# Optimization experiments

Hardware: AMD Instinct MI355X
Metric: run time of the kernel (lower is better)

Reference implementation:

```python
import jax, jax.numpy as jnp
import numpy as np
import math

N_QUBITS = 10
N_VQC_LAYERS = 3
N_ACTIONS = 3
B = 4096
T = 128
D = 1 << N_QUBITS
IU, JU = np.triu_indices(N_QUBITS, 1)  # combinations(range(N),2) order


def _ry(a):
    # [B] (or scalar) -> [...,2,2] complex64 RY(a)
    c, s = jnp.cos(a * 0.5), jnp.sin(a * 0.5)
    return jnp.stack([jnp.stack([c, -s], -1), jnp.stack([s, c], -1)], -2).astype(jnp.complex64)


def _rz(a):
    h = a.astype(jnp.complex64) * 0.5
    z = jnp.zeros_like(h)
    return jnp.stack([jnp.stack([jnp.exp(-1j * h), z], -1), jnp.stack([z, jnp.exp(1j * h)], -1)], -2)


def _rot(w):
    # Rot(phi,theta,omega) = RZ(omega) @ RY(theta) @ RZ(phi); w=[phi,theta,omega]
    return _rz(w[2]) @ _ry(w[1]) @ _rz(w[0])


def _apply_1q(state, gate, q, n):
    # apply 2x2 gate to qubit q of [B, 2^n] state (bit q has stride 2^(n-q-1))
    b, d = state.shape
    lo = 1 << (n - q - 1)
    hi = 1 << q
    s = state.reshape(b, hi, 2, lo)
    if gate.ndim == 3:
        s = jnp.einsum('bij,bhjl->bhil', gate, s)
    else:
        s = jnp.einsum('ij,bhjl->bhil', gate, s)
    return s.reshape(b, d)


def _static_tables(n, n_layers):
    s = np.arange(1 << n)
    # IsingZZ sign masks: +1 if bits differ, -1 if equal (matches torch buffer)
    masks = np.stack([
        np.where(((s >> (n - 1 - qi)) & 1) ^ ((s >> (n - 1 - qj)) & 1) == 1, 1.0, -1.0)
        for qi, qj in zip(IU, JU)
    ]).astype(np.float32)
    # PauliZ expectation signs per qubit
    zsigns = np.where(((s[None, :] >> (n - 1 - np.arange(n)[:, None])) & 1) == 0, 1.0, -1.0).astype(np.float32)
    # CNOT ring as index permutations (same math as the dense matmul in torch)
    perms = []
    for l in range(n_layers):
        rng = l % (n - 1) + 1 if n > 1 else 1
        layer = []
        for ctrl in range(n):
            tgt = (ctrl + rng) % n
            cb = (s >> (n - 1 - ctrl)) & 1
            layer.append(np.where(cb == 1, s ^ (1 << (n - 1 - tgt)), s))
        perms.append(layer)
    return masks, zsigns, perms


MASKS, ZSIGNS, PERMS = _static_tables(N_QUBITS, N_VQC_LAYERS)


def setup_inputs() -> dict:
    key = jax.random.key(0)
    k1, k2, k3, k4 = jax.random.split(key, 4)
    return {
        'c_kt': jax.random.normal(k1, (B, T, N_QUBITS), jnp.float32),
        'delta_c_kt': jax.random.normal(k2, (B, T, N_QUBITS), jnp.float32),
        'vqc_weights': jax.random.normal(k3, (N_VQC_LAYERS, N_QUBITS, 3), jnp.float32),
        'w_proj': jax.random.normal(k4, (N_ACTIONS, N_QUBITS), jnp.float32) / math.sqrt(N_QUBITS),
        'b_proj': jnp.zeros((N_ACTIONS,), jnp.float32),
        'log_alpha': jnp.zeros((), jnp.float32),
    }


def reference(c_kt, delta_c_kt, vqc_weights, w_proj, b_proj, log_alpha):
    n, L = N_QUBITS, N_VQC_LAYERS
    b, t, k_ = c_kt.shape
    # --- IsingCouplingEstimator: Pearson corr -> tanh(rho * alpha), zero diag ---
    feat = c_kt + 0.5 * delta_c_kt
    X = jnp.swapaxes(feat, 1, 2)                      # [B, K, T]
    Xc = X - X.mean(-1, keepdims=True)
    std = jnp.maximum(jnp.sqrt((Xc * Xc).sum(-1, keepdims=True) / (t - 1)), 1e-8)
    Xn = Xc / std
    rho = jnp.einsum('bit,bjt->bij', Xn, Xn) / (t - 1)
    rho = rho * (1.0 - jnp.eye(k_, dtype=rho.dtype))
    J = jnp.tanh(rho * jnp.exp(log_alpha))            # [B, K, K]
    j_upper = J[:, IU, JU]                            # [B, K*(K-1)/2]

    # --- angle encoding from last timestep ---
    theta = c_kt[:, -1, :]                            # [B, K]
    phi = delta_c_kt[:, -1, :]

    # --- TorchVQC state-vector simulation ---
    state = jnp.zeros((b, D), jnp.complex64).at[:, 0].set(1.0 + 0j)
    for q in range(n):
        state = _apply_1q(state, _ry(theta[:, q]), q, n)
        state = _apply_1q(state, _rz(phi[:, q]), q, n)
    # all IsingZZ phases fused: exp(0.5j * pi * sum_p J_p * mask_p)
    ang = math.pi * (j_upper @ jnp.asarray(MASKS))    # [B, D]
    state = state * jnp.exp(0.5j * ang.astype(jnp.complex64))
    for l in range(L):
        for q in range(n):
            state = _apply_1q(state, _rot(vqc_weights[l, q]), q, n)
        for q in range(n):
            state = state[:, PERMS[l][q]]             # CNOT as permutation
        if l < L - 1:                                 # data re-uploading
            for q in range(n):
                state = _apply_1q(state, _ry(theta[:, q] * 0.5), q, n)
                state = _apply_1q(state, _rz(phi[:, q] * 0.5), q, n)
    probs = jnp.real(state) ** 2 + jnp.imag(state) ** 2
    expvals = probs @ jnp.asarray(ZSIGNS).T           # [B, N] <Z_k>

    # --- logit projection ---
    return expvals @ w_proj.T + b_proj                # [B, n_actions]
```

## Files before the change

### kernel.cpp

```cpp
#include <hip/hip_runtime.h>


typedef float v2 __attribute__((ext_vector_type(2)));

template<int CTRL>
__device__ __forceinline__ float dppf(float v) {
  return __int_as_float(__builtin_amdgcn_update_dpp(
      0, __float_as_int(v), CTRL, 0xF, 0xF, true));
}

template<int LM>
__device__ __forceinline__ float xshfl(float v) {
  if constexpr (LM == 1) {
    return dppf<0xB1>(v);
  } else if constexpr (LM == 2) {
    return dppf<0x4E>(v);
  } else if constexpr (LM == 4) {
    return dppf<0x141>(dppf<0x1B>(v));
  } else if constexpr (LM == 8) {
    return dppf<0x128>(v);
  } else if constexpr (LM == 16) {
    return __int_as_float(__builtin_amdgcn_ds_swizzle(__float_as_int(v), 0x401F));
  } else {
    return __shfl_xor(v, 32);
  }
}

template<int LM>
__device__ __forceinline__ v2 xshfl2(v2 v) {
  v2 r; r.x = xshfl<LM>(v.x); r.y = xshfl<LM>(v.y); return r;
}

__device__ __forceinline__ float wred(float v) {
  v += xshfl<1>(v);
  v += xshfl<2>(v);
  v += xshfl<4>(v);
  v += xshfl<8>(v);
  v += xshfl<16>(v);
  v += xshfl<32>(v);
  return v;
}

__device__ __forceinline__ float rfl(float x) {
  return __int_as_float(__builtin_amdgcn_readfirstlane(__float_as_int(x)));
}

__device__ __forceinline__ float fast_tanh(float x) {
  return 1.0f - 2.0f / (__expf(2.0f * x) + 1.0f);
}

__device__ __forceinline__ v2 sneg(v2 a) {
  v2 r; r.x = -a.y; r.y = a.x; return r;
}

template<int BIT>
__device__ __forceinline__ void gate_apply(v2 (&st)[16], int lane,
    float m00r, float m00i, float m01r, float m01i,
    float m10r, float m10i, float m11r, float m11i) {
  if constexpr (BIT < 4) {
    #pragma unroll
    for (int r0 = 0; r0 < 16; ++r0) {
      if ((r0 & (1 << BIT)) == 0) {
        const int r1 = r0 | (1 << BIT);
        const v2 a0 = st[r0], a1 = st[r1];
        const v2 s0 = sneg(a0), s1 = sneg(a1);
        st[r0] = m00r*a0 + m00i*s0 + m01r*a1 + m01i*s1;
        st[r1] = m10r*a0 + m10i*s0 + m11r*a1 + m11i*s1;
      }
    }
  } else {
    constexpr int lm = 1 << (BIT - 4);
    const bool hi = (lane & lm) != 0;
    const float cAr = hi ? m11r : m00r, cAi = hi ? m11i : m00i;
    const float cBr = hi ? m10r : m01r, cBi = hi ? m10i : m01i;
    #pragma unroll
    for (int r = 0; r < 16; ++r) {
      const v2 p = xshfl2<lm>(st[r]);
      const v2 a = st[r];
      st[r] = cAr*a + cAi*sneg(a) + cBr*p + cBi*sneg(p);
    }
  }
}

template<int CB, int TB>
__device__ __forceinline__ void cnot_apply(v2 (&st)[16], int lane) {
  if constexpr (CB >= 4 && TB >= 4) {
    constexpr int lm = 1 << (TB - 4);
    const bool c1 = (lane & (1 << (CB - 4))) != 0;
    #pragma unroll
    for (int r = 0; r < 16; ++r) {
      const v2 p = xshfl2<lm>(st[r]);
      st[r].x = c1 ? p.x : st[r].x;
      st[r].y = c1 ? p.y : st[r].y;
    }
  } else if constexpr (CB >= 4 && TB < 4) {
    const bool c1 = (lane & (1 << (CB - 4))) != 0;
    #pragma unroll
    for (int r0 = 0; r0 < 16; ++r0) {
      if ((r0 & (1 << TB)) == 0) {
        const int r1 = r0 | (1 << TB);
        const v2 a = st[r0], b = st[r1];
        st[r0].x = c1 ? b.x : a.x;  st[r0].y = c1 ? b.y : a.y;
        st[r1].x = c1 ? a.x : b.x;  st[r1].y = c1 ? a.y : b.y;
      }
    }
  } else if constexpr (CB < 4 && TB >= 4) {
    constexpr int lm = 1 << (TB - 4);
    #pragma unroll
    for (int r = 0; r < 16; ++r) {
      if ((r & (1 << CB)) != 0) {
        st[r] = xshfl2<lm>(st[r]);
      }
    }
  } else {
    #pragma unroll
    for (int r0 = 0; r0 < 16; ++r0) {
      if ((r0 & (1 << CB)) != 0 && (r0 & (1 << TB)) == 0) {
        const int r1 = r0 | (1 << TB);
        const v2 t = st[r0]; st[r0] = st[r1]; st[r1] = t;
      }
    }
  }
}

template<int I, int J>
__device__ __forceinline__ void pair_accum(float t, int lane, float& Cc,
                                           float (&dcf)[4], float (&ecf)[6]) {
  if constexpr (J <= 5) {
    const bool diff = (((lane >> (5 - I)) ^ (lane >> (5 - J))) & 1) != 0;
    Cc += diff ? -t : t;
  } else if constexpr (I <= 5) {
    const bool b = ((lane >> (5 - I)) & 1) != 0;
    dcf[J - 6] += b ? -t : t;
  } else {
    constexpr int eb = (I == 6) ? 0 : (I == 7) ? 3 : 5;
    ecf[eb + (J - I - 1)] = rfl(t);
  }
}

#define PAIR(i, j) { \
  const v2 pr_ = ym[i] * ym[j]; \
  float dot_ = wred(pr_.x + pr_.y) * (1.0f/127.0f); \
  const float t_ = -1.5707963267948966f * fast_tanh(dot_ * expA); \
  pair_accum<i, j>(t_, lane, Cc, dcoef, ecoef); }

#define RLg(g_, x_) __int_as_float(__builtin_amdgcn_readlane(__float_as_int(x_), (g_)))

#define GATE(g_, q_) \
  gate_apply<9 - (q_)>(st, lane, \
      RLg(g_, Mr00), RLg(g_, Mi00), RLg(g_, Mr01), RLg(g_, Mi01), \
      RLg(g_, Mr10), RLg(g_, Mi10), RLg(g_, Mr11), RLg(g_, Mi11));

#define CNOT(ctrl, rng) cnot_apply<9 - (ctrl), 9 - ((((ctrl) + (rng)) % 10))>(st, lane);

extern "C" __global__ void __launch_bounds__(256, 2)
qhl_kernel(const float* __restrict__ c_kt, const float* __restrict__ dc_kt,
           const float* __restrict__ vw,  const float* __restrict__ w_proj,
           const float* __restrict__ b_proj, const float* __restrict__ log_alpha,
           float* __restrict__ out) {
  const int wave = threadIdx.x >> 6;
  const int lane = threadIdx.x & 63;
  const int bid  = blockIdx.x * 4 + wave;

  const float* c   = c_kt  + (size_t)bid * 1280;
  const float* dcp = dc_kt + (size_t)bid * 1280;

  float Mr00, Mi00, Mr01, Mi01, Mr10, Mi10, Mr11, Mi11;
  {
    const int g = lane < 30 ? lane : 0;
    const int l = g / 10, q = g - l * 10;
    const float w0 = vw[g*3+0], w1 = vw[g*3+1], w2 = vw[g*3+2];
    float cY, sY; __sincosf(0.5f*w1, &sY, &cY);
    float ca, sa; __sincosf(0.5f*(w0+w2), &sa, &ca);
    float cb, sb; __sincosf(0.5f*(w0-w2), &sb, &cb);
    const float r00r =  cY*ca, r00i = -cY*sa, r01r = -sY*cb, r01i = -sY*sb;
    const float r10r =  sY*cb, r10i = -sY*sb, r11r =  cY*ca, r11i =  cY*sa;
    if (l == 0) {
      Mr00 = r00r; Mi00 = r00i; Mr01 = r01r; Mi01 = r01i;
      Mr10 = r10r; Mi10 = r10i; Mr11 = r11r; Mi11 = r11i;
    } else {
      const float thq = c[1270 + q], phq = dcp[1270 + q];
      float cy, sy; __sincosf(0.25f * thq, &sy, &cy);
      float cz, sz; __sincosf(0.25f * phq, &sz, &cz);
      const float e00r =  cy*cz, e00i = -cy*sz, e01r = -sy*cz, e01i =  sy*sz;
      const float e10r =  sy*cz, e10i =  sy*sz, e11r =  cy*cz, e11i =  cy*sz;
      Mr00 = r00r*e00r - r00i*e00i + r01r*e10r - r01i*e10i;
      Mi00 = r00r*e00i + r00i*e00r + r01r*e10i + r01i*e10r;
      Mr01 = r00r*e01r - r00i*e01i + r01r*e11r - r01i*e11i;
      Mi01 = r00r*e01i + r00i*e01r + r01r*e11i + r01i*e11r;
      Mr10 = r10r*e00r - r10i*e00i + r11r*e10r - r11i*e10i;
      Mi10 = r10r*e00i + r10i*e00r + r11r*e10i + r11i*e10r;
      Mr11 = r10r*e01r - r10i*e01i + r11r*e11r - r11i*e11i;
      Mi11 = r10r*e01i + r10i*e01r + r11r*e11i + r11i*e11r;
    }
  }

  v2 ym[10];
  {
    const float2* c0 = (const float2*)(c   + lane * 10);
    const float2* d0 = (const float2*)(dcp + lane * 10);
    const float2* c1 = (const float2*)(c   + (lane + 64) * 10);
    const float2* d1 = (const float2*)(dcp + (lane + 64) * 10);
    #pragma unroll
    for (int k = 0; k < 5; ++k) {
      const float2 a0 = c0[k], b0 = d0[k], a1 = c1[k], b1 = d1[k];
      ym[2*k].x   = a0.x + 0.5f * b0.x;  ym[2*k].y   = a1.x + 0.5f * b1.x;
      ym[2*k+1].x = a0.y + 0.5f * b0.y;  ym[2*k+1].y = a1.y + 0.5f * b1.y;
    }
  }
  #pragma unroll
  for (int k = 0; k < 10; ++k) {
    const float mean = wred(ym[k].x + ym[k].y) * (1.0f / 128.0f);
    ym[k].x -= mean; ym[k].y -= mean;
    const v2 sq = ym[k] * ym[k];
    const float ss = wred(sq.x + sq.y);
    const float rs = fminf(__builtin_amdgcn_rsqf(ss * (1.0f / 127.0f)), 1e8f);
    ym[k] *= rs;
  }

  const float expA = rfl(__expf(log_alpha[0]));
  float Cc = 0.0f, dcoef[4] = {0, 0, 0, 0}, ecoef[6];
  PAIR(0,1) PAIR(0,2) PAIR(0,3) PAIR(0,4) PAIR(0,5) PAIR(0,6) PAIR(0,7) PAIR(0,8) PAIR(0,9)
  PAIR(1,2) PAIR(1,3) PAIR(1,4) PAIR(1,5) PAIR(1,6) PAIR(1,7) PAIR(1,8) PAIR(1,9)
  PAIR(2,3) PAIR(2,4) PAIR(2,5) PAIR(2,6) PAIR(2,7) PAIR(2,8) PAIR(2,9)
  PAIR(3,4) PAIR(3,5) PAIR(3,6) PAIR(3,7) PAIR(3,8) PAIR(3,9)
  PAIR(4,5) PAIR(4,6) PAIR(4,7) PAIR(4,8) PAIR(4,9)
  PAIR(5,6) PAIR(5,7) PAIR(5,8) PAIR(5,9)
  PAIR(6,7) PAIR(6,8) PAIR(6,9)
  PAIR(7,8) PAIR(7,9)
  PAIR(8,9)

  float th[10], ph[10];
  #pragma unroll
  for (int q = 0; q < 10; ++q) {
    th[q] = rfl(c[1270 + q]);
    ph[q] = rfl(dcp[1270 + q]);
  }

  v2 st[16];
  {
    v2 L; L.x = 1.0f; L.y = 0.0f;
    #pragma unroll
    for (int q = 0; q < 6; ++q) {
      float cy, sy; __sincosf(0.5f * th[q], &sy, &cy);
      float cz, sz; __sincosf(0.5f * ph[q], &sz, &cz);
      const bool b = ((lane >> (5 - q)) & 1) != 0;
      const float zr = b ? sy * cz : cy * cz;
      const float zi = b ? sy * sz : -cy * sz;
      L = zr * L + zi * sneg(L);
    }
    float ar[4][2], ai[4][2];
    #pragma unroll
    for (int t = 0; t < 4; ++t) {
      float cy, sy; __sincosf(0.5f * th[6 + t], &sy, &cy);
      float cz, sz; __sincosf(0.5f * ph[6 + t], &sz, &cz);
      ar[t][0] = rfl(cy * cz);  ai[t][0] = rfl(-cy * sz);
      ar[t][1] = rfl(sy * cz);  ai[t][1] = rfl( sy * sz);
    }
    #pragma unroll
    for (int r = 0; r < 16; ++r) {
      const int b3 = (r >> 3) & 1, b2 = (r >> 2) & 1, b1 = (r >> 1) & 1, b0 = r & 1;
      float Rr = ar[0][b3], Ri = ai[0][b3];
      float t1 = Rr * ar[1][b2] - Ri * ai[1][b2];
      Ri = Rr * ai[1][b2] + Ri * ar[1][b2]; Rr = t1;
      t1 = Rr * ar[2][b1] - Ri * ai[2][b1];
      Ri = Rr * ai[2][b1] + Ri * ar[2][b1]; Rr = t1;
      t1 = Rr * ar[3][b0] - Ri * ai[3][b0];
      Ri = Rr * ai[3][b0] + Ri * ar[3][b0]; Rr = t1;
      float h = Cc;
      h += b3 ? -dcoef[0] : dcoef[0];
      h += b2 ? -dcoef[1] : dcoef[1];
      h += b1 ? -dcoef[2] : dcoef[2];
      h += b0 ? -dcoef[3] : dcoef[3];
      h += (b3 ^ b2) ? -ecoef[0] : ecoef[0];
      h += (b3 ^ b1) ? -ecoef[1] : ecoef[1];
      h += (b3 ^ b0) ? -ecoef[2] : ecoef[2];
      h += (b2 ^ b1) ? -ecoef[3] : ecoef[3];
      h += (b2 ^ b0) ? -ecoef[4] : ecoef[4];
      h += (b1 ^ b0) ? -ecoef[5] : ecoef[5];
      float sn, cs; __sincosf(h, &sn, &cs);
      const v2 p = cs * L + sn * sneg(L);
      st[r] = Rr * p + Ri * sneg(p);
    }
  }

  GATE(0,0) GATE(1,1) GATE(2,2) GATE(3,3) GATE(4,4)
  GATE(5,5) GATE(6,6) GATE(7,7) GATE(8,8) GATE(9,9)
  CNOT(0,1) CNOT(1,1) CNOT(2,1) CNOT(3,1) CNOT(4,1)
  CNOT(5,1) CNOT(6,1) CNOT(7,1) CNOT(8,1) CNOT(9,1)
  GATE(10,0) GATE(11,1) GATE(12,2) GATE(13,3) GATE(14,4)
  GATE(15,5) GATE(16,6) GATE(17,7) GATE(18,8) GATE(19,9)
  CNOT(0,2) CNOT(1,2) CNOT(2,2) CNOT(3,2) CNOT(4,2)
  CNOT(5,2) CNOT(6,2) CNOT(7,2) CNOT(8,2) CNOT(9,2)
  GATE(20,0) GATE(21,1) GATE(22,2) GATE(23,3) GATE(24,4)
  GATE(25,5) GATE(26,6) GATE(27,7) GATE(28,8) GATE(29,9)
  CNOT(0,3) CNOT(1,3) CNOT(2,3) CNOT(3,3) CNOT(4,3)
  CNOT(5,3) CNOT(6,3) CNOT(7,3) CNOT(8,3) CNOT(9,3)

  float P = 0.0f, e6 = 0.0f, e7 = 0.0f, e8 = 0.0f, e9 = 0.0f;
  #pragma unroll
  for (int r = 0; r < 16; ++r) {
    const v2 sq = st[r] * st[r];
    const float pp = sq.x + sq.y;
    P  += pp;
    e6 += (r & 8) ? -pp : pp;
    e7 += (r & 4) ? -pp : pp;
    e8 += (r & 2) ? -pp : pp;
    e9 += (r & 1) ? -pp : pp;
  }
  float ev[10];
  ev[0] = (lane & 32) ? -P : P;
  ev[1] = (lane & 16) ? -P : P;
  ev[2] = (lane &  8) ? -P : P;
  ev[3] = (lane &  4) ? -P : P;
  ev[4] = (lane &  2) ? -P : P;
  ev[5] = (lane &  1) ? -P : P;
  ev[6] = e6; ev[7] = e7; ev[8] = e8; ev[9] = e9;
  #pragma unroll
  for (int i = 0; i < 10; ++i) ev[i] = wred(ev[i]);

  if (lane < 3) {
    float acc = b_proj[lane];
    #pragma unroll
    for (int i = 0; i < 10; ++i) acc += w_proj[lane * 10 + i] * ev[i];
    out[(size_t)bid * 3 + lane] = acc;
  }
}

extern "C" void kernel_launch(void* const* d_in, const int* in_sizes, int n_in,
                              void* d_out, int out_size, void* d_ws, size_t ws_size,
                              hipStream_t stream) {
  (void)in_sizes; (void)n_in; (void)d_ws; (void)ws_size; (void)out_size;
  const float* c_kt      = (const float*)d_in[0];
  const float* dc_kt     = (const float*)d_in[1];
  const float* vw        = (const float*)d_in[2];
  const float* w_proj    = (const float*)d_in[3];
  const float* b_proj    = (const float*)d_in[4];
  const float* log_alpha = (const float*)d_in[5];
  float* out = (float*)d_out;
  qhl_kernel<<<dim3(1024), dim3(256), 0, stream>>>(c_kt, dc_kt, vw, w_proj,
                                                   b_proj, log_alpha, out);
}
```

Baseline: 142.5 us.

## Replace per-value wave reductions with multi-value butterfly funnel reductions

Independent per-feature and per-pair wave reductions (10 means, 10 variances, 45 pair dot products, 10 expectation values) are replaced by a recursive-halving funnel. At each shuffle stage every lane sends half of its values and keeps the other half, so many sums are reduced at once with far fewer cross-lane operations. The tanh is then computed once per lane and the results are gathered with readlane. The per-row RY/RZ amplitude product for qubits 6-9 is also computed once per lane and broadcast, instead of being recomputed for all 16 rows. This adds select instructions and register pressure (a 48-float array) in exchange for much less shuffle traffic.

```diff
diff --git a/kernel.cpp b/kernel.cpp
--- a/kernel.cpp
+++ b/kernel.cpp
@@ -31,19 +31,49 @@
   v2 r; r.x = xshfl<LM>(v.x); r.y = xshfl<LM>(v.y); return r;
 }
 
-__device__ __forceinline__ float wred(float v) {
-  v += xshfl<1>(v);
-  v += xshfl<2>(v);
-  v += xshfl<4>(v);
-  v += xshfl<8>(v);
-  v += xshfl<16>(v);
-  v += xshfl<32>(v);
-  return v;
+template<int B, int NP>
+__device__ __forceinline__ void fstage(float* p, int lane) {
+  #pragma unroll
+  for (int i = 0; i < NP; ++i) {
+    const float send = (lane & B) ? p[i] : p[i + NP];
+    const float recv = xshfl<B>(send);
+    const float keep = (lane & B) ? p[i + NP] : p[i];
+    p[i] = keep + recv;
+  }
+}
+
+constexpr int holder_lane45(int v) {
+  const int a = v >= 24; int r = v - 24 * a;
+  const int b = r >= 12; r -= 12 * b;
+  const int c = r >= 6;  r -= 6 * c;
+  const int d = r >= 3;  r -= 3 * d;
+  const int e = r >= 2;  r -= 2 * e;
+  return a | (b << 1) | (c << 2) | (d << 3) | (e << 4) | (r << 5);
+}
+
+constexpr int holder_lane10(int v) {
+  const int a = v >= 5; int r = v - 5 * a;
+  const int b = r >= 3; r -= 3 * b;
+  const int c = r >= 2; r -= 2 * c;
+  return a | (b << 1) | (c << 2) | (r << 3);
+}
+
+__device__ __forceinline__ void funnel10(float* p, int lane) {
+  fstage<1, 5>(p, lane);
+  p[5] = 0.0f;
+  fstage<2, 3>(p, lane);
+  p[3] = 0.0f;
+  fstage<4, 2>(p, lane);
+  fstage<8, 1>(p, lane);
+  p[0] += xshfl<16>(p[0]);
+  p[0] += xshfl<32>(p[0]);
 }
 
 __device__ __forceinline__ float rfl(float x) {
   return __int_as_float(__builtin_amdgcn_readfirstlane(__float_as_int(x)));
 }
+
+#define RLg(g_, x_) __int_as_float(__builtin_amdgcn_readlane(__float_as_int(x_), (g_)))
 
 __device__ __forceinline__ float fast_tanh(float x) {
   return 1.0f - 2.0f / (__expf(2.0f * x) + 1.0f);
@@ -134,17 +164,11 @@
     dcf[J - 6] += b ? -t : t;
   } else {
     constexpr int eb = (I == 6) ? 0 : (I == 7) ? 3 : 5;
-    ecf[eb + (J - I - 1)] = rfl(t);
-  }
-}
-
-#define PAIR(i, j) { \
-  const v2 pr_ = ym[i] * ym[j]; \
-  float dot_ = wred(pr_.x + pr_.y) * (1.0f/127.0f); \
-  const float t_ = -1.5707963267948966f * fast_tanh(dot_ * expA); \
-  pair_accum<i, j>(t_, lane, Cc, dcoef, ecoef); }
-
-#define RLg(g_, x_) __int_as_float(__builtin_amdgcn_readlane(__float_as_int(x_), (g_)))
+    ecf[eb + (J - I - 1)] = t;
+  }
+}
+
+#define PACC(v_, i_, j_) pair_accum<i_, j_>(RLg(holder_lane45(v_), tl), lane, Cc, dcoef, ecoef);
 
 #define GATE(g_, q_) \
   gate_apply<9 - (q_)>(st, lane, \
@@ -208,33 +232,115 @@
       ym[2*k+1].x = a0.y + 0.5f * b0.y;  ym[2*k+1].y = a1.y + 0.5f * b1.y;
     }
   }
-  #pragma unroll
-  for (int k = 0; k < 10; ++k) {
-    const float mean = wred(ym[k].x + ym[k].y) * (1.0f / 128.0f);
-    ym[k].x -= mean; ym[k].y -= mean;
-    const v2 sq = ym[k] * ym[k];
-    const float ss = wred(sq.x + sq.y);
-    const float rs = fminf(__builtin_amdgcn_rsqf(ss * (1.0f / 127.0f)), 1e8f);
-    ym[k] *= rs;
+
+  {
+    float mb[6];
+    float m10[10];
+    #pragma unroll
+    for (int k = 0; k < 10; ++k) m10[k] = ym[k].x + ym[k].y;
+    #pragma unroll
+    for (int i = 0; i < 5; ++i) {
+      const float send = (lane & 1) ? m10[i] : m10[i + 5];
+      const float recv = xshfl<1>(send);
+      const float keep = (lane & 1) ? m10[i + 5] : m10[i];
+      mb[i] = keep + recv;
+    }
+    mb[5] = 0.0f;
+    fstage<2, 3>(mb, lane);
+    mb[3] = 0.0f;
+    fstage<4, 2>(mb, lane);
+    fstage<8, 1>(mb, lane);
+    mb[0] += xshfl<16>(mb[0]);
+    mb[0] += xshfl<32>(mb[0]);
+    mb[0] *= (1.0f / 128.0f);
+    #pragma unroll
+    for (int k = 0; k < 10; ++k) {
+      const float mk = RLg(holder_lane10(k), mb[0]);
+      ym[k].x -= mk; ym[k].y -= mk;
+    }
+    float s10[10];
+    #pragma unroll
+    for (int k = 0; k < 10; ++k) { const v2 sq = ym[k] * ym[k]; s10[k] = sq.x + sq.y; }
+    #pragma unroll
+    for (int i = 0; i < 5; ++i) {
+      const float send = (lane & 1) ? s10[i] : s10[i + 5];
+      const float recv = xshfl<1>(send);
+      const float keep = (lane & 1) ? s10[i + 5] : s10[i];
+      mb[i] = keep + recv;
+    }
+    mb[5] = 0.0f;
+    fstage<2, 3>(mb, lane);
+    mb[3] = 0.0f;
+    fstage<4, 2>(mb, lane);
+    fstage<8, 1>(mb, lane);
+    mb[0] += xshfl<16>(mb[0]);
+    mb[0] += xshfl<32>(mb[0]);
+    const float rsv = fminf(__builtin_amdgcn_rsqf(mb[0] * (1.0f / 127.0f)), 1e8f);
+    #pragma unroll
+    for (int k = 0; k < 10; ++k) {
+      const float rk = RLg(holder_lane10(k), rsv);
+      ym[k].x *= rk; ym[k].y *= rk;
+    }
   }
 
   const float expA = rfl(__expf(log_alpha[0]));
   float Cc = 0.0f, dcoef[4] = {0, 0, 0, 0}, ecoef[6];
-  PAIR(0,1) PAIR(0,2) PAIR(0,3) PAIR(0,4) PAIR(0,5) PAIR(0,6) PAIR(0,7) PAIR(0,8) PAIR(0,9)
-  PAIR(1,2) PAIR(1,3) PAIR(1,4) PAIR(1,5) PAIR(1,6) PAIR(1,7) PAIR(1,8) PAIR(1,9)
-  PAIR(2,3) PAIR(2,4) PAIR(2,5) PAIR(2,6) PAIR(2,7) PAIR(2,8) PAIR(2,9)
-  PAIR(3,4) PAIR(3,5) PAIR(3,6) PAIR(3,7) PAIR(3,8) PAIR(3,9)
-  PAIR(4,5) PAIR(4,6) PAIR(4,7) PAIR(4,8) PAIR(4,9)
-  PAIR(5,6) PAIR(5,7) PAIR(5,8) PAIR(5,9)
-  PAIR(6,7) PAIR(6,8) PAIR(6,9)
-  PAIR(7,8) PAIR(7,9)
-  PAIR(8,9)
+  float tl;
+  {
+    constexpr int PI_[45] = {0,0,0,0,0,0,0,0,0, 1,1,1,1,1,1,1,1, 2,2,2,2,2,2,2,
+                             3,3,3,3,3,3, 4,4,4,4,4, 5,5,5,5, 6,6,6, 7,7, 8};
+    constexpr int PJ_[45] = {1,2,3,4,5,6,7,8,9, 2,3,4,5,6,7,8,9, 3,4,5,6,7,8,9,
+                             4,5,6,7,8,9, 5,6,7,8,9, 6,7,8,9, 7,8,9, 8,9, 9};
+    float p[48];
+    #pragma unroll
+    for (int v = 0; v < 45; ++v) {
+      const v2 pr = ym[PI_[v]] * ym[PJ_[v]];
+      p[v] = pr.x + pr.y;
+    }
+    p[45] = 0.0f; p[46] = 0.0f; p[47] = 0.0f;
+    fstage<1, 24>(p, lane);
+    fstage<2, 12>(p, lane);
+    fstage<4, 6>(p, lane);
+    fstage<8, 3>(p, lane);
+    p[3] = 0.0f;
+    fstage<16, 2>(p, lane);
+    fstage<32, 1>(p, lane);
+    const float sc = expA * (1.0f / 127.0f);
+    tl = -1.5707963267948966f * fast_tanh(p[0] * sc);
+  }
+  PACC(0,0,1) PACC(1,0,2) PACC(2,0,3) PACC(3,0,4) PACC(4,0,5) PACC(5,0,6) PACC(6,0,7) PACC(7,0,8) PACC(8,0,9)
+  PACC(9,1,2) PACC(10,1,3) PACC(11,1,4) PACC(12,1,5) PACC(13,1,6) PACC(14,1,7) PACC(15,1,8) PACC(16,1,9)
+  PACC(17,2,3) PACC(18,2,4) PACC(19,2,5) PACC(20,2,6) PACC(21,2,7) PACC(22,2,8) PACC(23,2,9)
+  PACC(24,3,4) PACC(25,3,5) PACC(26,3,6) PACC(27,3,7) PACC(28,3,8) PACC(29,3,9)
+  PACC(30,4,5) PACC(31,4,6) PACC(32,4,7) PACC(33,4,8) PACC(34,4,9)
+  PACC(35,5,6) PACC(36,5,7) PACC(37,5,8) PACC(38,5,9)
+  PACC(39,6,7) PACC(40,6,8) PACC(41,6,9)
+  PACC(42,7,8) PACC(43,7,9)
+  PACC(44,8,9)
 
   float th[10], ph[10];
   #pragma unroll
   for (int q = 0; q < 10; ++q) {
     th[q] = rfl(c[1270 + q]);
     ph[q] = rfl(dcp[1270 + q]);
+  }
+
+  float Rr_l, Ri_l;
+  {
+    const int rr = lane & 15;
+    float prr = 1.0f, pri = 0.0f;
+    #pragma unroll
+    for (int t = 0; t < 4; ++t) {
+      float cy, sy; __sincosf(0.5f * th[6 + t], &sy, &cy);
+      float cz, sz; __sincosf(0.5f * ph[6 + t], &sz, &cz);
+      const bool b = ((rr >> (3 - t)) & 1) != 0;
+      const float fr = b ? sy * cz : cy * cz;
+      const float fi = b ? sy * sz : -cy * sz;
+      const float nr = prr * fr - pri * fi;
+      pri = prr * fi + pri * fr;
+      prr = nr;
+    }
+    Rr_l = prr; Ri_l = pri;
   }
 
   v2 st[16];
@@ -249,24 +355,11 @@
       const float zi = b ? sy * sz : -cy * sz;
       L = zr * L + zi * sneg(L);
     }
-    float ar[4][2], ai[4][2];
-    #pragma unroll
-    for (int t = 0; t < 4; ++t) {
-      float cy, sy; __sincosf(0.5f * th[6 + t], &sy, &cy);
-      float cz, sz; __sincosf(0.5f * ph[6 + t], &sz, &cz);
-      ar[t][0] = rfl(cy * cz);  ai[t][0] = rfl(-cy * sz);
-      ar[t][1] = rfl(sy * cz);  ai[t][1] = rfl( sy * sz);
-    }
     #pragma unroll
     for (int r = 0; r < 16; ++r) {
       const int b3 = (r >> 3) & 1, b2 = (r >> 2) & 1, b1 = (r >> 1) & 1, b0 = r & 1;
-      float Rr = ar[0][b3], Ri = ai[0][b3];
-      float t1 = Rr * ar[1][b2] - Ri * ai[1][b2];
-      Ri = Rr * ai[1][b2] + Ri * ar[1][b2]; Rr = t1;
-      t1 = Rr * ar[2][b1] - Ri * ai[2][b1];
-      Ri = Rr * ai[2][b1] + Ri * ar[2][b1]; Rr = t1;
-      t1 = Rr * ar[3][b0] - Ri * ai[3][b0];
-      Ri = Rr * ai[3][b0] + Ri * ar[3][b0]; Rr = t1;
+      const float Rr = RLg(r, Rr_l);
+      const float Ri = RLg(r, Ri_l);
       float h = Cc;
       h += b3 ? -dcoef[0] : dcoef[0];
       h += b2 ? -dcoef[1] : dcoef[1];
@@ -308,22 +401,39 @@
     e8 += (r & 2) ? -pp : pp;
     e9 += (r & 1) ? -pp : pp;
   }
-  float ev[10];
-  ev[0] = (lane & 32) ? -P : P;
-  ev[1] = (lane & 16) ? -P : P;
-  ev[2] = (lane &  8) ? -P : P;
-  ev[3] = (lane &  4) ? -P : P;
-  ev[4] = (lane &  2) ? -P : P;
-  ev[5] = (lane &  1) ? -P : P;
-  ev[6] = e6; ev[7] = e7; ev[8] = e8; ev[9] = e9;
-  #pragma unroll
-  for (int i = 0; i < 10; ++i) ev[i] = wred(ev[i]);
-
-  if (lane < 3) {
-    float acc = b_proj[lane];
-    #pragma unroll
-    for (int i = 0; i < 10; ++i) acc += w_proj[lane * 10 + i] * ev[i];
-    out[(size_t)bid * 3 + lane] = acc;
+  float mv[10];
+  mv[0] = (lane & 32) ? -P : P;
+  mv[1] = (lane & 16) ? -P : P;
+  mv[2] = (lane &  8) ? -P : P;
+  mv[3] = (lane &  4) ? -P : P;
+  mv[4] = (lane &  2) ? -P : P;
+  mv[5] = (lane &  1) ? -P : P;
+  mv[6] = e6; mv[7] = e7; mv[8] = e8; mv[9] = e9;
+  {
+    float fb[6];
+    #pragma unroll
+    for (int i = 0; i < 5; ++i) {
+      const float send = (lane & 1) ? mv[i] : mv[i + 5];
+      const float recv = xshfl<1>(send);
+      const float keep = (lane & 1) ? mv[i + 5] : mv[i];
+      fb[i] = keep + recv;
+    }
+    fb[5] = 0.0f;
+    fstage<2, 3>(fb, lane);
+    fb[3] = 0.0f;
+    fstage<4, 2>(fb, lane);
+    fstage<8, 1>(fb, lane);
+    fb[0] += xshfl<16>(fb[0]);
+    fb[0] += xshfl<32>(fb[0]);
+    float ev[10];
+    #pragma unroll
+    for (int k = 0; k < 10; ++k) ev[k] = RLg(holder_lane10(k), fb[0]);
+    if (lane < 3) {
+      float acc = b_proj[lane];
+      #pragma unroll
+      for (int i = 0; i < 10; ++i) acc += w_proj[lane * 10 + i] * ev[i];
+      out[(size_t)bid * 3 + lane] = acc;
+    }
   }
 }
 
```

Result: faster. 131.0 us (-8.1%).
